# Kernel tuning notes

Measured on AMD Instinct MI355X. Metric: run time of the kernel, lower is better.

The kernel has to match this reference:

```python
import jax, jax.numpy as jnp
import numpy as np

B, L, C = 8, 4096, 512
WS, SHIFT, H = 64, 32, 16
HD = C // H
HID = 4 * C


def _ln(x, w, b):
    m = x.mean(-1, keepdims=True)
    v = ((x - m) ** 2).mean(-1, keepdims=True)
    return (x - m) / jnp.sqrt(v + 1e-5) * w + b


def _attn_mask():
    # 0 / -100 mask for shifted windows, shape (nW, WS, WS)
    img = np.zeros((L,), np.float32)
    cnt = 0
    for s in (slice(0, L - WS), slice(L - WS, L - SHIFT), slice(L - SHIFT, L)):
        img[s] = cnt
        cnt += 1
    mw = img.reshape(L // WS, WS)
    d = mw[:, :, None] - mw[:, None, :]
    return jnp.asarray(np.where(d != 0, -100.0, 0.0).astype(np.float32))


def _cpb_coords():
    # log-spaced continuous relative coords, shape (2*WS-1, 1)
    r = np.arange(-(WS - 1), WS, dtype=np.float32) / (WS - 1) * 8.0
    t = np.sign(r) * np.log2(np.abs(r) + 1.0) / np.log2(8.0)
    return jnp.asarray(t[:, None].astype(np.float32))


def _rel_index():
    c = np.arange(WS)
    return jnp.asarray((c[:, None] - c[None, :] + WS - 1).astype(np.int32))


def setup_inputs():
    key = jax.random.key(0)
    ks = jax.random.split(key, 8)
    n = jax.random.normal
    return {
        "x": n(ks[0], (B, L, C), jnp.float32),
        "qkv_w": n(ks[1], (3 * C, C), jnp.float32) * 0.02,
        "q_bias": jnp.zeros((C,), jnp.float32),
        "v_bias": jnp.zeros((C,), jnp.float32),
        "logit_scale": jnp.log(10.0 * jnp.ones((H, 1, 1), jnp.float32)),
        "cpb_w1": n(ks[2], (512, 1), jnp.float32) * 0.02,
        "cpb_b1": jnp.zeros((512,), jnp.float32),
        "cpb_w2": n(ks[3], (H, 512), jnp.float32) * 0.02,
        "proj_w": n(ks[4], (C, C), jnp.float32) * 0.02,
        "proj_b": jnp.zeros((C,), jnp.float32),
        "norm1_w": jnp.ones((C,), jnp.float32),
        "norm1_b": jnp.zeros((C,), jnp.float32),
        "norm2_w": jnp.ones((C,), jnp.float32),
        "norm2_b": jnp.zeros((C,), jnp.float32),
        "fc1_w": n(ks[5], (HID, C), jnp.float32) * 0.02,
        "fc1_b": jnp.zeros((HID,), jnp.float32),
        "fc2_w": n(ks[6], (C, HID), jnp.float32) * 0.02,
        "fc2_b": jnp.zeros((C,), jnp.float32),
    }


def reference(x, qkv_w, q_bias, v_bias, logit_scale, cpb_w1, cpb_b1, cpb_w2,
              proj_w, proj_b, norm1_w, norm1_b, norm2_w, norm2_b,
              fc1_w, fc1_b, fc2_w, fc2_b):
    nW = L // WS
    shortcut = x
    # cyclic shift + window partition
    xs = jnp.roll(x, -SHIFT, axis=1)
    xw = xs.reshape(B * nW, WS, C)
    # qkv with q/v bias only (k bias is zero)
    qkv_b = jnp.concatenate([q_bias, jnp.zeros_like(v_bias), v_bias])
    qkv = (xw @ qkv_w.T + qkv_b).reshape(B * nW, WS, 3, H, HD)
    qkv = qkv.transpose(2, 0, 3, 1, 4)  # (3, B*nW, H, WS, HD)
    q, k, v = qkv[0], qkv[1], qkv[2]
    # cosine attention with learned, clamped per-head temperature
    qn = q / jnp.maximum(jnp.linalg.norm(q, axis=-1, keepdims=True), 1e-12)
    kn = k / jnp.maximum(jnp.linalg.norm(k, axis=-1, keepdims=True), 1e-12)
    attn = jnp.einsum('whnd,whmd->whnm', qn, kn)
    scale = jnp.exp(jnp.minimum(logit_scale, jnp.log(100.0)))  # (H,1,1)
    attn = attn * scale
    # continuous relative position bias via small MLP
    tbl = jax.nn.relu(_cpb_coords() @ cpb_w1.T + cpb_b1) @ cpb_w2.T  # (2WS-1, H)
    bias = tbl[_rel_index()]  # (WS, WS, H)
    bias = 16.0 * jax.nn.sigmoid(bias.transpose(2, 0, 1))  # (H, WS, WS)
    attn = attn + bias[None]
    # shift mask (0 / -100), per window
    mask = _attn_mask()  # (nW, WS, WS)
    attn = attn.reshape(B, nW, H, WS, WS) + mask[None, :, None]
    attn = jax.nn.softmax(attn.reshape(B * nW, H, WS, WS), axis=-1)
    out = jnp.einsum('whnm,whmd->whnd', attn, v)
    out = out.transpose(0, 2, 1, 3).reshape(B * nW, WS, C)
    out = out @ proj_w.T + proj_b
    # window reverse + reverse shift
    out = jnp.roll(out.reshape(B, L, C), SHIFT, axis=1)
    # Swin v2 post-norm residuals
    x1 = shortcut + _ln(out, norm1_w, norm1_b)
    h = jax.nn.gelu(x1 @ fc1_w.T + fc1_b, approximate=False) @ fc2_w.T + fc2_b
    return x1 + _ln(h, norm2_w, norm2_b)
```

## Files before the change

### kernel.cpp

```cpp
#include <hip/hip_runtime.h>
#include <hip/hip_bf16.h>
#include <math.h>

typedef unsigned short u16;
typedef __bf16 bf16x8 __attribute__((ext_vector_type(8)));
typedef float f32x4 __attribute__((ext_vector_type(4)));
typedef unsigned short u16x8 __attribute__((ext_vector_type(8)));
typedef unsigned short u16x4 __attribute__((ext_vector_type(4)));
typedef unsigned short u16x2 __attribute__((ext_vector_type(2)));

#define DEV static __device__ __forceinline__

DEV float b2f(u16 v) { unsigned u = ((unsigned)v) << 16; return __builtin_bit_cast(float, u); }
DEV u16 f2bf(float f) {
  unsigned u = __builtin_bit_cast(unsigned, f);
  u += 0x7fffu + ((u >> 16) & 1u);
  return (u16)(u >> 16);
}

DEV void async16(const void* g, void* l) {
  __builtin_amdgcn_global_load_lds(
      (const __attribute__((address_space(1))) void*)g,
      (__attribute__((address_space(3))) void*)l, 16, 0, 0);
}

__global__ __launch_bounds__(256) void cvt_all_kernel(
    const float* __restrict__ x,  const float* __restrict__ wq,
    const float* __restrict__ wp, const float* __restrict__ w1,
    const float* __restrict__ w2,
    u16* __restrict__ dx, u16* __restrict__ dq, u16* __restrict__ dp,
    u16* __restrict__ d1, u16* __restrict__ d2)
{
  const int i = blockIdx.x * 256 + threadIdx.x;
  const float* s; u16* d; int off;
  if (i < 4194304)      { s = x;  d = dx; off = i; }
  else if (i < 4390912) { s = wq; d = dq; off = i - 4194304; }
  else if (i < 4456448) { s = wp; d = dp; off = i - 4390912; }
  else if (i < 4718592) { s = w1; d = d1; off = i - 4456448; }
  else if (i < 4980736) { s = w2; d = d2; off = i - 4718592; }
  else return;
  float4 v = ((const float4*)s)[off];
  u16x4 o;
  o[0] = f2bf(v.x); o[1] = f2bf(v.y); o[2] = f2bf(v.z); o[3] = f2bf(v.w);
  ((u16x4*)d)[off] = o;
}

__global__ __launch_bounds__(64) void cpb1_kernel(
    const float* __restrict__ w1, const float* __restrict__ b1,
    const float* __restrict__ w2, float* __restrict__ tbl)
{
  const int r = blockIdx.x, h = blockIdx.y;
  const int lane = threadIdx.x;
  float rv = (float)(r - 63) * (8.0f / 63.0f);
  float sgn = (rv > 0.f) ? 1.f : ((rv < 0.f) ? -1.f : 0.f);
  float t = sgn * log2f(fabsf(rv) + 1.f) * (1.f / 3.f);
  float part = 0.f;
  for (int k = lane; k < 512; k += 64) {
    float hid = fmaxf(t * w1[k] + b1[k], 0.f);
    part += hid * w2[h * 512 + k];
  }
  #pragma unroll
  for (int o = 32; o > 0; o >>= 1) part += __shfl_down(part, o);
  if (lane == 0) tbl[r * 16 + h] = part;
}

__global__ __launch_bounds__(256) void cpb2_kernel(
    const float* __restrict__ tbl, float* __restrict__ btbl)
{
  const int h = blockIdx.x;
  for (int idx = threadIdx.x; idx < 4096; idx += 256) {
    int i = idx >> 6, j = idx & 63;
    float v = tbl[(i - j + 63) * 16 + h];
    btbl[h * 4096 + idx] = 16.f / (1.f + __expf(-v));
  }
}

template <int MODE>
__global__ __launch_bounds__(512, 2) void gemm_bt(
    const u16* __restrict__ A, const u16* __restrict__ W,
    const float* __restrict__ bias1, const float* __restrict__ bias2,
    u16* __restrict__ out, int nby, int N, int K)
{
  extern __shared__ __attribute__((aligned(16))) u16 smem[];
  const int tid = threadIdx.x;
  const int lane = tid & 63;
  const int wv = tid >> 6;
  const int q8 = (int)gridDim.x >> 3;
  const int swb = (blockIdx.x & 7) * q8 + (blockIdx.x >> 3);
  const int m0 = (swb / nby) * 256;
  const int n0 = (swb % nby) * 256;
  const int wm = (wv >> 2) * 128;
  const int wn = (wv & 3) * 64;
  const int fr = lane & 15;
  const int hi = lane >> 4;
  const int srow = tid >> 3;
  const int kb = (tid & 7) ^ (srow & 7);
  f32x4 acc[8][4] = {};

  auto stageA = [&](int buf, int k0, int i) {
    const int r = srow + (i << 6);
    const u16* src;
    if constexpr (MODE == 0) {
      const int mg = m0 + r;
      const int bb = mg >> 12;
      const int p = mg & 4095;
      const long ga = ((long)bb << 12) + ((p + 32) & 4095);
      src = A + ga * (long)K + k0 + kb * 8;
    } else if constexpr (MODE == 1) {
      const int kk = k0 + kb * 8;
      src = A + (size_t)(kk >> 5) * 1048576 + (size_t)(m0 + r) * 32 + (kk & 31);
    } else {
      src = A + (size_t)(m0 + r) * K + k0 + kb * 8;
    }
    async16(src, smem + buf * 16384 + ((i << 9) + tid) * 8);
  };
  auto stageB = [&](int buf, int k0, int i) {
    const int r = srow + (i << 6);
    async16(W + (size_t)(n0 + r) * K + k0 + kb * 8,
            smem + 32768 + buf * 16384 + ((i << 9) + tid) * 8);
  };
  auto stage_part = [&](int buf, int k0, int part) {
    if (part == 0)      { stageB(buf, k0, 0); stageB(buf, k0, 1); }
    else if (part == 1) { stageB(buf, k0, 2); stageB(buf, k0, 3); }
    else if (part == 2) { stageA(buf, k0, 0); stageA(buf, k0, 2); }
    else                { stageA(buf, k0, 1); stageA(buf, k0, 3); }
  };

  auto phase_compute = [&](const u16* lac, const u16* lbc, int mh, int ks) {
    bf16x8 fa[4], fb[4];
    const int sw = hi + (ks << 2);
    #pragma unroll
    for (int mi = 0; mi < 4; ++mi) {
      const int r = wm + ((mh << 2) + mi) * 16 + fr;
      fa[mi] = *(const bf16x8*)&lac[r * 64 + ((sw ^ (r & 7)) << 3)];
    }
    #pragma unroll
    for (int ni = 0; ni < 4; ++ni) {
      const int r = wn + ni * 16 + fr;
      fb[ni] = *(const bf16x8*)&lbc[r * 64 + ((sw ^ (r & 7)) << 3)];
    }
    asm volatile("s_waitcnt lgkmcnt(0)" ::: "memory");
    __builtin_amdgcn_sched_barrier(0);
    __builtin_amdgcn_s_setprio(1);
    #pragma unroll
    for (int mi = 0; mi < 4; ++mi)
      #pragma unroll
      for (int ni = 0; ni < 4; ++ni)
        acc[(mh << 2) + mi][ni] = __builtin_amdgcn_mfma_f32_16x16x32_bf16(
            fa[mi], fb[ni], acc[(mh << 2) + mi][ni], 0, 0, 0);
    __builtin_amdgcn_s_setprio(0);
  };

  const int NT = K >> 6;
  stage_part(0, 0, 0); stage_part(0, 0, 1); stage_part(0, 0, 2); stage_part(0, 0, 3);
  int cur = 0;
  for (int kt = 0; kt < NT; ++kt) {
    const bool hn = (kt + 1) < NT;
    const int nk0 = (kt + 1) << 6;
    const u16* lac = smem + cur * 16384;
    const u16* lbc = smem + 32768 + cur * 16384;
    const int nb = cur ^ 1;
    asm volatile("s_waitcnt vmcnt(2)" ::: "memory");
    __builtin_amdgcn_s_barrier();
    if (hn) stage_part(nb, nk0, 0);
    phase_compute(lac, lbc, 0, 0);
    if (hn) { asm volatile("s_waitcnt vmcnt(2)" ::: "memory"); }
    else    { asm volatile("s_waitcnt vmcnt(0)" ::: "memory"); }
    __builtin_amdgcn_s_barrier();
    if (hn) stage_part(nb, nk0, 1);
    phase_compute(lac, lbc, 1, 0);
    if (hn) stage_part(nb, nk0, 2);
    phase_compute(lac, lbc, 0, 1);
    if (hn) stage_part(nb, nk0, 3);
    phase_compute(lac, lbc, 1, 1);
    cur ^= 1;
  }

  const int lrow = hi * 4;
  #pragma unroll
  for (int mi = 0; mi < 8; ++mi) {
    #pragma unroll
    for (int ni = 0; ni < 4; ++ni) {
      const int n = n0 + wn + ni * 16 + fr;
      #pragma unroll
      for (int r = 0; r < 4; ++r) {
        const int m = m0 + wm + mi * 16 + lrow + r;
        float v = acc[mi][ni][r];
        if constexpr (MODE == 0) {
          const int which = n >> 9, c = n & 511;
          const int hh = c >> 5, d = c & 31;
          float bias = (which == 0) ? bias1[c] : (which == 2 ? bias2[c] : 0.f);
          const int g = m >> 6, ii = m & 63;
          out[(size_t)which * 16777216 + (size_t)g * 32768 + hh * 2048 + ii * 32 + d] =
              f2bf(v + bias);
        } else if constexpr (MODE == 2) {
          float t = v + bias1[n];
          float u = t * t;
          float z = t * (1.5957691216f + 0.0713548163f * u);
          float ge = t / (1.f + __expf(-z));
          out[(size_t)m * N + n] = f2bf(ge);
        } else {
          out[(size_t)m * N + n] = f2bf(v + bias1[n]);
        }
      }
    }
  }
}

__global__ __launch_bounds__(256) void gemm_sm3(
    const u16* __restrict__ A, const u16* __restrict__ W,
    const float* __restrict__ bias1,
    u16* __restrict__ out, int nby, int N, int K)
{
  __shared__ __attribute__((aligned(16))) u16 lA[2][8192];
  __shared__ __attribute__((aligned(16))) u16 lB[2][8192];
  const int tid = threadIdx.x;
  const int wid = tid >> 6;
  const int lane = tid & 63;
  const int q8 = (int)gridDim.x >> 3;
  const int swb = (blockIdx.x & 7) * q8 + (blockIdx.x >> 3);
  const int m0 = (swb / nby) * 128;
  const int n0 = (swb % nby) * 128;
  const int wm = (wid >> 1) * 64;
  const int wn = (wid & 1) * 64;
  f32x4 acc[4][4] = {};

  const int srow8 = lane >> 3;
  const int kel = ((lane & 7) ^ srow8) * 8;

  auto stage = [&](int b, int k0) {
    #pragma unroll
    for (int cc = 0; cc < 4; ++cc) {
      const int rb = wid * 32 + cc * 8;
      const int r = rb + srow8;
      async16(A + (size_t)(m0 + r) * K + k0 + kel, &lA[b][rb * 64]);
      async16(W + (size_t)(n0 + r) * K + k0 + kel, &lB[b][rb * 64]);
    }
  };

  const int NT = K >> 6;
  stage(0, 0);
  __syncthreads();
  int cur = 0;
  const int fr = lane & 15;
  const int hi = lane >> 4;
  const int fsw = fr & 7;
  for (int kt = 0; kt < NT; ++kt) {
    if (kt + 1 < NT) stage(cur ^ 1, (kt + 1) << 6);
    #pragma unroll
    for (int ks = 0; ks < 2; ++ks) {
      bf16x8 fa[4], fb[4];
      #pragma unroll
      for (int t = 0; t < 4; ++t) {
        const int ra = wm + t * 16 + fr;
        fa[t] = *(const bf16x8*)&lA[cur][ra * 64 + (((hi + 4 * ks) ^ fsw) << 3)];
        const int rbq = wn + t * 16 + fr;
        fb[t] = *(const bf16x8*)&lB[cur][rbq * 64 + (((hi + 4 * ks) ^ fsw) << 3)];
      }
      #pragma unroll
      for (int mi = 0; mi < 4; ++mi)
        #pragma unroll
        for (int ni = 0; ni < 4; ++ni)
          acc[mi][ni] = __builtin_amdgcn_mfma_f32_16x16x32_bf16(fa[mi], fb[ni], acc[mi][ni], 0, 0, 0);
    }
    __syncthreads();
    cur ^= 1;
  }

  const int lrow = (lane >> 4) * 4;
  #pragma unroll
  for (int mi = 0; mi < 4; ++mi)
    #pragma unroll
    for (int ni = 0; ni < 4; ++ni) {
      const int n = n0 + wn + ni * 16 + fr;
      #pragma unroll
      for (int r = 0; r < 4; ++r) {
        const int m = m0 + wm + mi * 16 + lrow + r;
        out[(size_t)m * N + n] = f2bf(acc[mi][ni][r] + bias1[n]);
      }
    }
}

__global__ __launch_bounds__(256) void attn_kernel(
    const u16* __restrict__ qkv, const float* __restrict__ ls,
    const float* __restrict__ btbl, u16* __restrict__ attnT)
{
  const int gg = blockIdx.x;
  const int w = threadIdx.x >> 6;
  const int lane = threadIdx.x & 63;
  __shared__ __attribute__((aligned(16))) u16 vt[4][2048];
  __shared__ __attribute__((aligned(16))) u16 pl[4][4096];
  const bool maskw = ((gg & 63) == 63);
  const int fr = lane & 15;
  const int fkq = (lane >> 4) * 8;
  const int crow = (lane >> 4) * 4;

  for (int t = 0; t < 4; ++t) {
    const int h = w * 4 + t;
    const size_t bgh = (size_t)gg * 32768 + (size_t)h * 2048;

    {
      const u16x8* vp = (const u16x8*)(qkv + 33554432 + bgh + (size_t)lane * 32);
      #pragma unroll
      for (int c = 0; c < 4; ++c) {
        u16x8 vr = vp[c];
        #pragma unroll
        for (int e = 0; e < 8; ++e) {
          const int d = c * 8 + e;
          const int addr = d * 64 + (((lane >> 3) ^ (d & 7)) << 3) + (lane & 7);
          vt[w][addr] = vr[e];
        }
      }
    }

    const float scale = __expf(fminf(ls[h], 4.6051701859880914f));
    bf16x8 qa[4], kb[4];
    #pragma unroll
    for (int mi = 0; mi < 4; ++mi) {
      u16x8 raw = *(const u16x8*)(qkv + bgh + (size_t)(mi * 16 + fr) * 32 + fkq);
      float f[8]; float ssum = 0.f;
      #pragma unroll
      for (int e = 0; e < 8; ++e) { f[e] = b2f(raw[e]); ssum += f[e] * f[e]; }
      ssum += __shfl_xor(ssum, 16); ssum += __shfl_xor(ssum, 32);
      const float mul = scale / fmaxf(sqrtf(ssum), 1e-12f);
      u16x8 tmp;
      #pragma unroll
      for (int e = 0; e < 8; ++e) tmp[e] = f2bf(f[e] * mul);
      qa[mi] = __builtin_bit_cast(bf16x8, tmp);
    }
    #pragma unroll
    for (int ni = 0; ni < 4; ++ni) {
      u16x8 raw = *(const u16x8*)(qkv + 16777216 + bgh + (size_t)(ni * 16 + fr) * 32 + fkq);
      float f[8]; float ssum = 0.f;
      #pragma unroll
      for (int e = 0; e < 8; ++e) { f[e] = b2f(raw[e]); ssum += f[e] * f[e]; }
      ssum += __shfl_xor(ssum, 16); ssum += __shfl_xor(ssum, 32);
      const float mul = 1.f / fmaxf(sqrtf(ssum), 1e-12f);
      u16x8 tmp;
      #pragma unroll
      for (int e = 0; e < 8; ++e) tmp[e] = f2bf(f[e] * mul);
      kb[ni] = __builtin_bit_cast(bf16x8, tmp);
    }

    f32x4 s[4][4] = {};
    __builtin_amdgcn_s_setprio(1);
    #pragma unroll
    for (int mi = 0; mi < 4; ++mi)
      #pragma unroll
      for (int ni = 0; ni < 4; ++ni)
        s[mi][ni] = __builtin_amdgcn_mfma_f32_16x16x32_bf16(qa[mi], kb[ni], s[mi][ni], 0, 0, 0);
    __builtin_amdgcn_s_setprio(0);

    const float mh = scale + 16.f;
    float inv_[4][4];
    #pragma unroll
    for (int mi = 0; mi < 4; ++mi) {
      #pragma unroll
      for (int r = 0; r < 4; ++r) {
        const int row = mi * 16 + crow + r;
        float es = 0.f;
        #pragma unroll
        for (int ni = 0; ni < 4; ++ni) {
          const int col = ni * 16 + fr;
          float sv = s[mi][ni][r] + btbl[h * 4096 + row * 64 + col];
          if (maskw && ((row < 32) != (col < 32))) sv -= 100.f;
          const float e = __expf(sv - mh);
          s[mi][ni][r] = e;
          es += e;
        }
        es += __shfl_xor(es, 1); es += __shfl_xor(es, 2);
        es += __shfl_xor(es, 4); es += __shfl_xor(es, 8);
        inv_[mi][r] = 1.f / fmaxf(es, 1e-37f);
      }
    }

    #pragma unroll
    for (int mi = 0; mi < 4; ++mi)
      #pragma unroll
      for (int r = 0; r < 4; ++r) {
        const int row = mi * 16 + crow + r;
        #pragma unroll
        for (int ni = 0; ni < 4; ++ni) {
          const int col = ni * 16 + fr;
          const int addr = row * 64 + (((col >> 3) ^ (row & 7)) << 3) + (col & 7);
          pl[w][addr] = f2bf(s[mi][ni][r]);
        }
      }
    __syncthreads();

    f32x4 o[4][2] = {};
    #pragma unroll
    for (int ks = 0; ks < 2; ++ks) {
      bf16x8 vbf[2];
      #pragma unroll
      for (int np = 0; np < 2; ++np) {
        const int d = np * 16 + fr;
        const int jb = (lane >> 4) + ks * 4;
        vbf[np] = *(const bf16x8*)&vt[w][d * 64 + ((jb ^ (d & 7)) << 3)];
      }
      __builtin_amdgcn_s_setprio(1);
      #pragma unroll
      for (int mp = 0; mp < 4; ++mp) {
        const int row = mp * 16 + fr;
        const int cb = (lane >> 4) + ks * 4;
        bf16x8 paf = *(const bf16x8*)&pl[w][row * 64 + ((cb ^ (row & 7)) << 3)];
        o[mp][0] = __builtin_amdgcn_mfma_f32_16x16x32_bf16(paf, vbf[0], o[mp][0], 0, 0, 0);
        o[mp][1] = __builtin_amdgcn_mfma_f32_16x16x32_bf16(paf, vbf[1], o[mp][1], 0, 0, 0);
      }
      __builtin_amdgcn_s_setprio(0);
    }

    #pragma unroll
    for (int mp = 0; mp < 4; ++mp)
      #pragma unroll
      for (int r = 0; r < 4; ++r) {
        const int row = mp * 16 + crow + r;
        const float iv = inv_[mp][r];
        u16* op = attnT + (size_t)h * 1048576 + (size_t)(gg * 64 + row) * 32;
        op[fr]      = f2bf(o[mp][0][r] * iv);
        op[16 + fr] = f2bf(o[mp][1][r] * iv);
      }
    __syncthreads();
  }
}

__global__ __launch_bounds__(256) void ln1_kernel(
    const u16* __restrict__ proj, const float* __restrict__ x,
    const float* __restrict__ w, const float* __restrict__ bb,
    u16* __restrict__ x1h)
{
  const int t = blockIdx.x;
  const int b = t >> 12, l = t & 4095;
  const int p = (l - 32) & 4095;
  const size_t srow = (((size_t)b << 12) + p) << 9;
  const int c0 = threadIdx.x * 2;
  u16x2 pv = *(const u16x2*)(proj + srow + c0);
  float v0 = b2f(pv[0]), v1 = b2f(pv[1]);
  float s = v0 + v1, ss = v0 * v0 + v1 * v1;
  #pragma unroll
  for (int o = 32; o > 0; o >>= 1) { s += __shfl_down(s, o); ss += __shfl_down(ss, o); }
  __shared__ float red[8];
  const int wid = threadIdx.x >> 6, lane = threadIdx.x & 63;
  if (lane == 0) { red[wid] = s; red[4 + wid] = ss; }
  __syncthreads();
  const float S = red[0] + red[1] + red[2] + red[3];
  const float SS = red[4] + red[5] + red[6] + red[7];
  const float mean = S * (1.f / 512.f);
  const float var = SS * (1.f / 512.f) - mean * mean;
  const float rstd = rsqrtf(var + 1e-5f);
  const size_t orow = (size_t)t << 9;
  float2 xv = *(const float2*)(x + orow + c0);
  const float r0 = xv.x + (v0 - mean) * rstd * w[c0] + bb[c0];
  const float r1 = xv.y + (v1 - mean) * rstd * w[c0 + 1] + bb[c0 + 1];
  u16x2 ho; ho[0] = f2bf(r0); ho[1] = f2bf(r1);
  *(u16x2*)(x1h + orow + c0) = ho;
}

__global__ __launch_bounds__(256) void ln2_kernel(
    const u16* __restrict__ fc2, const u16* __restrict__ x1h,
    const float* __restrict__ w, const float* __restrict__ bb,
    float* __restrict__ out)
{
  const int t = blockIdx.x;
  const size_t row = (size_t)t << 9;
  const int c0 = threadIdx.x * 2;
  u16x2 pv = *(const u16x2*)(fc2 + row + c0);
  float v0 = b2f(pv[0]), v1 = b2f(pv[1]);
  float s = v0 + v1, ss = v0 * v0 + v1 * v1;
  #pragma unroll
  for (int o = 32; o > 0; o >>= 1) { s += __shfl_down(s, o); ss += __shfl_down(ss, o); }
  __shared__ float red[8];
  const int wid = threadIdx.x >> 6, lane = threadIdx.x & 63;
  if (lane == 0) { red[wid] = s; red[4 + wid] = ss; }
  __syncthreads();
  const float S = red[0] + red[1] + red[2] + red[3];
  const float SS = red[4] + red[5] + red[6] + red[7];
  const float mean = S * (1.f / 512.f);
  const float var = SS * (1.f / 512.f) - mean * mean;
  const float rstd = rsqrtf(var + 1e-5f);
  u16x2 xv = *(const u16x2*)(x1h + row + c0);
  const float r0 = b2f(xv[0]) + (v0 - mean) * rstd * w[c0] + bb[c0];
  const float r1 = b2f(xv[1]) + (v1 - mean) * rstd * w[c0 + 1] + bb[c0 + 1];
  float2 fo; fo.x = r0; fo.y = r1;
  *(float2*)(out + row + c0) = fo;
}

extern "C" void kernel_launch(void* const* d_in, const int* in_sizes, int n_in,
                              void* d_out, int out_size, void* d_ws, size_t ws_size,
                              hipStream_t stream) {
  const float* x        = (const float*)d_in[0];
  const float* qkv_w    = (const float*)d_in[1];
  const float* q_bias   = (const float*)d_in[2];
  const float* v_bias   = (const float*)d_in[3];
  const float* lscale   = (const float*)d_in[4];
  const float* cpb_w1   = (const float*)d_in[5];
  const float* cpb_b1   = (const float*)d_in[6];
  const float* cpb_w2   = (const float*)d_in[7];
  const float* proj_w   = (const float*)d_in[8];
  const float* proj_b   = (const float*)d_in[9];
  const float* n1w      = (const float*)d_in[10];
  const float* n1b      = (const float*)d_in[11];
  const float* n2w      = (const float*)d_in[12];
  const float* n2b      = (const float*)d_in[13];
  const float* fc1_w    = (const float*)d_in[14];
  const float* fc1_b    = (const float*)d_in[15];
  const float* fc2_w    = (const float*)d_in[16];
  const float* fc2_b    = (const float*)d_in[17];

  if (ws_size < 134217728u) return;
  char* ws = (char*)d_ws;
  u16* wqkv   = (u16*)(ws + 0);
  u16* wproj  = (u16*)(ws + 1572864);
  u16* wfc1   = (u16*)(ws + 2097152);
  u16* wfc2   = (u16*)(ws + 4194304);
  float* btbl = (float*)(ws + 6291456);
  u16* qkv    = (u16*)(ws + 6553600);
  u16* projo  = (u16*)(ws + 6553600);
  u16* hbuf   = (u16*)(ws + 6553600);
  u16* fc2oh  = (u16*)(ws + 73662464);
  u16* x1h    = (u16*)(ws + 94371840);
  float* tbl  = (float*)(ws + 127926272);
  u16* xbf   = (u16*)d_out;
  u16* attnT = (u16*)d_out;
  float* out = (float*)d_out;

  hipFuncSetAttribute((const void*)gemm_bt<0>, hipFuncAttributeMaxDynamicSharedMemorySize, 131072);
  hipFuncSetAttribute((const void*)gemm_bt<1>, hipFuncAttributeMaxDynamicSharedMemorySize, 131072);
  hipFuncSetAttribute((const void*)gemm_bt<2>, hipFuncAttributeMaxDynamicSharedMemorySize, 131072);

  cvt_all_kernel<<<19456, 256, 0, stream>>>(
      x, qkv_w, proj_w, fc1_w, fc2_w, xbf, wqkv, wproj, wfc1, wfc2);
  cpb1_kernel<<<dim3(127, 16), 64, 0, stream>>>(cpb_w1, cpb_b1, cpb_w2, tbl);
  cpb2_kernel<<<16, 256, 0, stream>>>(tbl, btbl);

  gemm_bt<0><<<768, 512, 131072, stream>>>(
      xbf, wqkv, q_bias, v_bias, qkv, 6, 1536, 512);
  attn_kernel<<<512, 256, 0, stream>>>(qkv, lscale, btbl, attnT);
  gemm_bt<1><<<256, 512, 131072, stream>>>(
      attnT, wproj, proj_b, nullptr, projo, 2, 512, 512);
  ln1_kernel<<<32768, 256, 0, stream>>>(projo, x, n1w, n1b, x1h);
  for (int half = 0; half < 2; ++half) {
    const u16* a2 = x1h + (size_t)half * 8388608;
    gemm_bt<2><<<512, 512, 131072, stream>>>(
        a2, wfc1, fc1_b, nullptr, hbuf, 8, 2048, 512);
    gemm_sm3<<<512, 256, 0, stream>>>(
        hbuf, wfc2, fc2_b, fc2oh, 4, 512, 2048);
    ln2_kernel<<<16384, 256, 0, stream>>>(
        fc2oh, a2, n2w, n2b, out + (size_t)half * 8388608);
  }
}
```

Baseline: 442.2 us.

## Replace all GEMMs with single-buffer 128x128 tile kernel and vectorize layernorms

Drops the 256x256 double-buffered, phase-pipelined GEMM and the separate fc2 kernel. All four GEMMs now use one simple 128x128, K=32 step kernel with static LDS and two barriers per step, which targets higher occupancy. Both layernorm kernels now handle one row per wavefront with 8-element vector loads and shuffle reductions, removing the LDS reduction and block barrier. The GEMMs lose software pipelining and data reuse, so global load latency is exposed on every K step.

```diff
diff --git a/kernel.cpp b/kernel.cpp
--- a/kernel.cpp
+++ b/kernel.cpp
@@ -76,109 +76,68 @@
 }
 
 template <int MODE>
-__global__ __launch_bounds__(512, 2) void gemm_bt(
+__global__ __launch_bounds__(256, 4) void gemm_m97(
     const u16* __restrict__ A, const u16* __restrict__ W,
     const float* __restrict__ bias1, const float* __restrict__ bias2,
     u16* __restrict__ out, int nby, int N, int K)
 {
-  extern __shared__ __attribute__((aligned(16))) u16 smem[];
+  __shared__ __attribute__((aligned(16))) u16 lA[4096];
+  __shared__ __attribute__((aligned(16))) u16 lB[4096];
   const int tid = threadIdx.x;
   const int lane = tid & 63;
   const int wv = tid >> 6;
   const int q8 = (int)gridDim.x >> 3;
   const int swb = (blockIdx.x & 7) * q8 + (blockIdx.x >> 3);
-  const int m0 = (swb / nby) * 256;
-  const int n0 = (swb % nby) * 256;
-  const int wm = (wv >> 2) * 128;
-  const int wn = (wv & 3) * 64;
+  const int m0 = (swb / nby) * 128;
+  const int n0 = (swb % nby) * 128;
+  const int wm = (wv >> 1) * 64;
+  const int wn = (wv & 1) * 64;
   const int fr = lane & 15;
   const int hi = lane >> 4;
-  const int srow = tid >> 3;
-  const int kb = (tid & 7) ^ (srow & 7);
-  f32x4 acc[8][4] = {};
-
-  auto stageA = [&](int buf, int k0, int i) {
-    const int r = srow + (i << 6);
-    const u16* src;
-    if constexpr (MODE == 0) {
-      const int mg = m0 + r;
-      const int bb = mg >> 12;
-      const int p = mg & 4095;
-      const long ga = ((long)bb << 12) + ((p + 32) & 4095);
-      src = A + ga * (long)K + k0 + kb * 8;
-    } else if constexpr (MODE == 1) {
-      const int kk = k0 + kb * 8;
-      src = A + (size_t)(kk >> 5) * 1048576 + (size_t)(m0 + r) * 32 + (kk & 31);
-    } else {
-      src = A + (size_t)(m0 + r) * K + k0 + kb * 8;
-    }
-    async16(src, smem + buf * 16384 + ((i << 9) + tid) * 8);
-  };
-  auto stageB = [&](int buf, int k0, int i) {
-    const int r = srow + (i << 6);
-    async16(W + (size_t)(n0 + r) * K + k0 + kb * 8,
-            smem + 32768 + buf * 16384 + ((i << 9) + tid) * 8);
-  };
-  auto stage_part = [&](int buf, int k0, int part) {
-    if (part == 0)      { stageB(buf, k0, 0); stageB(buf, k0, 1); }
-    else if (part == 1) { stageB(buf, k0, 2); stageB(buf, k0, 3); }
-    else if (part == 2) { stageA(buf, k0, 0); stageA(buf, k0, 2); }
-    else                { stageA(buf, k0, 1); stageA(buf, k0, 3); }
-  };
-
-  auto phase_compute = [&](const u16* lac, const u16* lbc, int mh, int ks) {
+  const int sr = tid >> 2;
+  const int sp = tid & 3;
+  f32x4 acc[4][4] = {};
+
+  for (int k0 = 0; k0 < K; k0 += 32) {
+    #pragma unroll
+    for (int i = 0; i < 2; ++i) {
+      const int r = i * 64 + sr;
+      const int kk = k0 + ((sp ^ ((r >> 1) & 3)) << 3);
+      const u16* asrc;
+      if constexpr (MODE == 0) {
+        const int mg = m0 + r;
+        const int bb = mg >> 12;
+        const int p = mg & 4095;
+        const long ga = ((long)bb << 12) + ((p + 32) & 4095);
+        asrc = A + ga * (long)K + kk;
+      } else if constexpr (MODE == 1) {
+        asrc = A + (size_t)(kk >> 5) * 1048576 + (size_t)(m0 + r) * 32 + (kk & 31);
+      } else {
+        asrc = A + (size_t)(m0 + r) * K + kk;
+      }
+      async16(asrc, lA + r * 32 + sp * 8);
+      async16(W + (size_t)(n0 + r) * K + kk, lB + r * 32 + sp * 8);
+    }
+    __syncthreads();
     bf16x8 fa[4], fb[4];
-    const int sw = hi + (ks << 2);
-    #pragma unroll
-    for (int mi = 0; mi < 4; ++mi) {
-      const int r = wm + ((mh << 2) + mi) * 16 + fr;
-      fa[mi] = *(const bf16x8*)&lac[r * 64 + ((sw ^ (r & 7)) << 3)];
-    }
-    #pragma unroll
-    for (int ni = 0; ni < 4; ++ni) {
-      const int r = wn + ni * 16 + fr;
-      fb[ni] = *(const bf16x8*)&lbc[r * 64 + ((sw ^ (r & 7)) << 3)];
-    }
-    asm volatile("s_waitcnt lgkmcnt(0)" ::: "memory");
-    __builtin_amdgcn_sched_barrier(0);
-    __builtin_amdgcn_s_setprio(1);
+    #pragma unroll
+    for (int t = 0; t < 4; ++t) {
+      const int ra = wm + t * 16 + fr;
+      fa[t] = *(const bf16x8*)&lA[ra * 32 + ((hi ^ ((ra >> 1) & 3)) << 3)];
+      const int rb = wn + t * 16 + fr;
+      fb[t] = *(const bf16x8*)&lB[rb * 32 + ((hi ^ ((rb >> 1) & 3)) << 3)];
+    }
     #pragma unroll
     for (int mi = 0; mi < 4; ++mi)
       #pragma unroll
       for (int ni = 0; ni < 4; ++ni)
-        acc[(mh << 2) + mi][ni] = __builtin_amdgcn_mfma_f32_16x16x32_bf16(
-            fa[mi], fb[ni], acc[(mh << 2) + mi][ni], 0, 0, 0);
-    __builtin_amdgcn_s_setprio(0);
-  };
-
-  const int NT = K >> 6;
-  stage_part(0, 0, 0); stage_part(0, 0, 1); stage_part(0, 0, 2); stage_part(0, 0, 3);
-  int cur = 0;
-  for (int kt = 0; kt < NT; ++kt) {
-    const bool hn = (kt + 1) < NT;
-    const int nk0 = (kt + 1) << 6;
-    const u16* lac = smem + cur * 16384;
-    const u16* lbc = smem + 32768 + cur * 16384;
-    const int nb = cur ^ 1;
-    asm volatile("s_waitcnt vmcnt(2)" ::: "memory");
-    __builtin_amdgcn_s_barrier();
-    if (hn) stage_part(nb, nk0, 0);
-    phase_compute(lac, lbc, 0, 0);
-    if (hn) { asm volatile("s_waitcnt vmcnt(2)" ::: "memory"); }
-    else    { asm volatile("s_waitcnt vmcnt(0)" ::: "memory"); }
-    __builtin_amdgcn_s_barrier();
-    if (hn) stage_part(nb, nk0, 1);
-    phase_compute(lac, lbc, 1, 0);
-    if (hn) stage_part(nb, nk0, 2);
-    phase_compute(lac, lbc, 0, 1);
-    if (hn) stage_part(nb, nk0, 3);
-    phase_compute(lac, lbc, 1, 1);
-    cur ^= 1;
+        acc[mi][ni] = __builtin_amdgcn_mfma_f32_16x16x32_bf16(fa[mi], fb[ni], acc[mi][ni], 0, 0, 0);
+    __syncthreads();
   }
 
   const int lrow = hi * 4;
   #pragma unroll
-  for (int mi = 0; mi < 8; ++mi) {
+  for (int mi = 0; mi < 4; ++mi) {
     #pragma unroll
     for (int ni = 0; ni < 4; ++ni) {
       const int n = n0 + wn + ni * 16 + fr;
@@ -189,7 +148,7 @@
         if constexpr (MODE == 0) {
           const int which = n >> 9, c = n & 511;
           const int hh = c >> 5, d = c & 31;
-          float bias = (which == 0) ? bias1[c] : (which == 2 ? bias2[c] : 0.f);
+          const float bias = (which == 0) ? bias1[c] : (which == 2 ? bias2[c] : 0.f);
           const int g = m >> 6, ii = m & 63;
           out[(size_t)which * 16777216 + (size_t)g * 32768 + hh * 2048 + ii * 32 + d] =
               f2bf(v + bias);
@@ -205,80 +164,6 @@
       }
     }
   }
-}
-
-__global__ __launch_bounds__(256) void gemm_sm3(
-    const u16* __restrict__ A, const u16* __restrict__ W,
-    const float* __restrict__ bias1,
-    u16* __restrict__ out, int nby, int N, int K)
-{
-  __shared__ __attribute__((aligned(16))) u16 lA[2][8192];
-  __shared__ __attribute__((aligned(16))) u16 lB[2][8192];
-  const int tid = threadIdx.x;
-  const int wid = tid >> 6;
-  const int lane = tid & 63;
-  const int q8 = (int)gridDim.x >> 3;
-  const int swb = (blockIdx.x & 7) * q8 + (blockIdx.x >> 3);
-  const int m0 = (swb / nby) * 128;
-  const int n0 = (swb % nby) * 128;
-  const int wm = (wid >> 1) * 64;
-  const int wn = (wid & 1) * 64;
-  f32x4 acc[4][4] = {};
-
-  const int srow8 = lane >> 3;
-  const int kel = ((lane & 7) ^ srow8) * 8;
-
-  auto stage = [&](int b, int k0) {
-    #pragma unroll
-    for (int cc = 0; cc < 4; ++cc) {
-      const int rb = wid * 32 + cc * 8;
-      const int r = rb + srow8;
-      async16(A + (size_t)(m0 + r) * K + k0 + kel, &lA[b][rb * 64]);
-      async16(W + (size_t)(n0 + r) * K + k0 + kel, &lB[b][rb * 64]);
-    }
-  };
-
-  const int NT = K >> 6;
-  stage(0, 0);
-  __syncthreads();
-  int cur = 0;
-  const int fr = lane & 15;
-  const int hi = lane >> 4;
-  const int fsw = fr & 7;
-  for (int kt = 0; kt < NT; ++kt) {
-    if (kt + 1 < NT) stage(cur ^ 1, (kt + 1) << 6);
-    #pragma unroll
-    for (int ks = 0; ks < 2; ++ks) {
-      bf16x8 fa[4], fb[4];
-      #pragma unroll
-      for (int t = 0; t < 4; ++t) {
-        const int ra = wm + t * 16 + fr;
-        fa[t] = *(const bf16x8*)&lA[cur][ra * 64 + (((hi + 4 * ks) ^ fsw) << 3)];
-        const int rbq = wn + t * 16 + fr;
-        fb[t] = *(const bf16x8*)&lB[cur][rbq * 64 + (((hi + 4 * ks) ^ fsw) << 3)];
-      }
-      #pragma unroll
-      for (int mi = 0; mi < 4; ++mi)
-        #pragma unroll
-        for (int ni = 0; ni < 4; ++ni)
-          acc[mi][ni] = __builtin_amdgcn_mfma_f32_16x16x32_bf16(fa[mi], fb[ni], acc[mi][ni], 0, 0, 0);
-    }
-    __syncthreads();
-    cur ^= 1;
-  }
-
-  const int lrow = (lane >> 4) * 4;
-  #pragma unroll
-  for (int mi = 0; mi < 4; ++mi)
-    #pragma unroll
-    for (int ni = 0; ni < 4; ++ni) {
-      const int n = n0 + wn + ni * 16 + fr;
-      #pragma unroll
-      for (int r = 0; r < 4; ++r) {
-        const int m = m0 + wm + mi * 16 + lrow + r;
-        out[(size_t)m * N + n] = f2bf(acc[mi][ni][r] + bias1[n]);
-      }
-    }
 }
 
 __global__ __launch_bounds__(256) void attn_kernel(
@@ -429,31 +314,30 @@
     const float* __restrict__ w, const float* __restrict__ bb,
     u16* __restrict__ x1h)
 {
-  const int t = blockIdx.x;
-  const int b = t >> 12, l = t & 4095;
+  const int row = blockIdx.x * 4 + (threadIdx.x >> 6);
+  const int lane = threadIdx.x & 63;
+  const int b = row >> 12, l = row & 4095;
   const int p = (l - 32) & 4095;
   const size_t srow = (((size_t)b << 12) + p) << 9;
-  const int c0 = threadIdx.x * 2;
-  u16x2 pv = *(const u16x2*)(proj + srow + c0);
-  float v0 = b2f(pv[0]), v1 = b2f(pv[1]);
-  float s = v0 + v1, ss = v0 * v0 + v1 * v1;
-  #pragma unroll
-  for (int o = 32; o > 0; o >>= 1) { s += __shfl_down(s, o); ss += __shfl_down(ss, o); }
-  __shared__ float red[8];
-  const int wid = threadIdx.x >> 6, lane = threadIdx.x & 63;
-  if (lane == 0) { red[wid] = s; red[4 + wid] = ss; }
-  __syncthreads();
-  const float S = red[0] + red[1] + red[2] + red[3];
-  const float SS = red[4] + red[5] + red[6] + red[7];
-  const float mean = S * (1.f / 512.f);
-  const float var = SS * (1.f / 512.f) - mean * mean;
+  const int c0 = lane * 8;
+  u16x8 pv = *(const u16x8*)(proj + srow + c0);
+  float v[8]; float s = 0.f, ss = 0.f;
+  #pragma unroll
+  for (int e = 0; e < 8; ++e) { v[e] = b2f(pv[e]); s += v[e]; ss += v[e] * v[e]; }
+  #pragma unroll
+  for (int o = 32; o > 0; o >>= 1) { s += __shfl_xor(s, o); ss += __shfl_xor(ss, o); }
+  const float mean = s * (1.f / 512.f);
+  const float var = ss * (1.f / 512.f) - mean * mean;
   const float rstd = rsqrtf(var + 1e-5f);
-  const size_t orow = (size_t)t << 9;
-  float2 xv = *(const float2*)(x + orow + c0);
-  const float r0 = xv.x + (v0 - mean) * rstd * w[c0] + bb[c0];
-  const float r1 = xv.y + (v1 - mean) * rstd * w[c0 + 1] + bb[c0 + 1];
-  u16x2 ho; ho[0] = f2bf(r0); ho[1] = f2bf(r1);
-  *(u16x2*)(x1h + orow + c0) = ho;
+  const size_t orow = (size_t)row << 9;
+  float4 x0 = *(const float4*)(x + orow + c0);
+  float4 x1 = *(const float4*)(x + orow + c0 + 4);
+  const float xs[8] = {x0.x, x0.y, x0.z, x0.w, x1.x, x1.y, x1.z, x1.w};
+  u16x8 ho;
+  #pragma unroll
+  for (int e = 0; e < 8; ++e)
+    ho[e] = f2bf(xs[e] + (v[e] - mean) * rstd * w[c0 + e] + bb[c0 + e]);
+  *(u16x8*)(x1h + orow + c0) = ho;
 }
 
 __global__ __launch_bounds__(256) void ln2_kernel(
@@ -461,28 +345,29 @@
     const float* __restrict__ w, const float* __restrict__ bb,
     float* __restrict__ out)
 {
-  const int t = blockIdx.x;
-  const size_t row = (size_t)t << 9;
-  const int c0 = threadIdx.x * 2;
-  u16x2 pv = *(const u16x2*)(fc2 + row + c0);
-  float v0 = b2f(pv[0]), v1 = b2f(pv[1]);
-  float s = v0 + v1, ss = v0 * v0 + v1 * v1;
-  #pragma unroll
-  for (int o = 32; o > 0; o >>= 1) { s += __shfl_down(s, o); ss += __shfl_down(ss, o); }
-  __shared__ float red[8];
-  const int wid = threadIdx.x >> 6, lane = threadIdx.x & 63;
-  if (lane == 0) { red[wid] = s; red[4 + wid] = ss; }
-  __syncthreads();
-  const float S = red[0] + red[1] + red[2] + red[3];
-  const float SS = red[4] + red[5] + red[6] + red[7];
-  const float mean = S * (1.f / 512.f);
-  const float var = SS * (1.f / 512.f) - mean * mean;
+  const int row = blockIdx.x * 4 + (threadIdx.x >> 6);
+  const int lane = threadIdx.x & 63;
+  const size_t r512 = (size_t)row << 9;
+  const int c0 = lane * 8;
+  u16x8 pv = *(const u16x8*)(fc2 + r512 + c0);
+  float v[8]; float s = 0.f, ss = 0.f;
+  #pragma unroll
+  for (int e = 0; e < 8; ++e) { v[e] = b2f(pv[e]); s += v[e]; ss += v[e] * v[e]; }
+  #pragma unroll
+  for (int o = 32; o > 0; o >>= 1) { s += __shfl_xor(s, o); ss += __shfl_xor(ss, o); }
+  const float mean = s * (1.f / 512.f);
+  const float var = ss * (1.f / 512.f) - mean * mean;
   const float rstd = rsqrtf(var + 1e-5f);
-  u16x2 xv = *(const u16x2*)(x1h + row + c0);
-  const float r0 = b2f(xv[0]) + (v0 - mean) * rstd * w[c0] + bb[c0];
-  const float r1 = b2f(xv[1]) + (v1 - mean) * rstd * w[c0 + 1] + bb[c0 + 1];
-  float2 fo; fo.x = r0; fo.y = r1;
-  *(float2*)(out + row + c0) = fo;
+  u16x8 xv = *(const u16x8*)(x1h + r512 + c0);
+  float4 o0, o1;
+  float r[8];
+  #pragma unroll
+  for (int e = 0; e < 8; ++e)
+    r[e] = b2f(xv[e]) + (v[e] - mean) * rstd * w[c0 + e] + bb[c0 + e];
+  o0.x = r[0]; o0.y = r[1]; o0.z = r[2]; o0.w = r[3];
+  o1.x = r[4]; o1.y = r[5]; o1.z = r[6]; o1.w = r[7];
+  *(float4*)(out + r512 + c0) = o0;
+  *(float4*)(out + r512 + c0 + 4) = o1;
 }
 
 extern "C" void kernel_launch(void* const* d_in, const int* in_sizes, int n_in,
@@ -524,28 +409,24 @@
   u16* attnT = (u16*)d_out;
   float* out = (float*)d_out;
 
-  hipFuncSetAttribute((const void*)gemm_bt<0>, hipFuncAttributeMaxDynamicSharedMemorySize, 131072);
-  hipFuncSetAttribute((const void*)gemm_bt<1>, hipFuncAttributeMaxDynamicSharedMemorySize, 131072);
-  hipFuncSetAttribute((const void*)gemm_bt<2>, hipFuncAttributeMaxDynamicSharedMemorySize, 131072);
-
   cvt_all_kernel<<<19456, 256, 0, stream>>>(
       x, qkv_w, proj_w, fc1_w, fc2_w, xbf, wqkv, wproj, wfc1, wfc2);
   cpb1_kernel<<<dim3(127, 16), 64, 0, stream>>>(cpb_w1, cpb_b1, cpb_w2, tbl);
   cpb2_kernel<<<16, 256, 0, stream>>>(tbl, btbl);
 
-  gemm_bt<0><<<768, 512, 131072, stream>>>(
-      xbf, wqkv, q_bias, v_bias, qkv, 6, 1536, 512);
+  gemm_m97<0><<<3072, 256, 0, stream>>>(
+      xbf, wqkv, q_bias, v_bias, qkv, 12, 1536, 512);
   attn_kernel<<<512, 256, 0, stream>>>(qkv, lscale, btbl, attnT);
-  gemm_bt<1><<<256, 512, 131072, stream>>>(
-      attnT, wproj, proj_b, nullptr, projo, 2, 512, 512);
-  ln1_kernel<<<32768, 256, 0, stream>>>(projo, x, n1w, n1b, x1h);
+  gemm_m97<1><<<1024, 256, 0, stream>>>(
+      attnT, wproj, proj_b, nullptr, projo, 4, 512, 512);
+  ln1_kernel<<<8192, 256, 0, stream>>>(projo, x, n1w, n1b, x1h);
   for (int half = 0; half < 2; ++half) {
     const u16* a2 = x1h + (size_t)half * 8388608;
-    gemm_bt<2><<<512, 512, 131072, stream>>>(
-        a2, wfc1, fc1_b, nullptr, hbuf, 8, 2048, 512);
-    gemm_sm3<<<512, 256, 0, stream>>>(
-        hbuf, wfc2, fc2_b, fc2oh, 4, 512, 2048);
-    ln2_kernel<<<16384, 256, 0, stream>>>(
+    gemm_m97<2><<<2048, 256, 0, stream>>>(
+        a2, wfc1, fc1_b, nullptr, hbuf, 16, 2048, 512);
+    gemm_m97<3><<<512, 256, 0, stream>>>(
+        hbuf, wfc2, fc2_b, nullptr, fc2oh, 4, 512, 2048);
+    ln2_kernel<<<4096, 256, 0, stream>>>(
         fc2oh, a2, n2w, n2b, out + (size_t)half * 8388608);
   }
 }
```

After: 451.7 us. +2.1%, slower.
